# Performance work log

Measured on AMD Instinct MI355X. Metric: run time of the kernel, lower is better.

## Reference

```python
import jax, jax.numpy as jnp
import numpy as np

OUT_FEATURES = 4096
IN_FEATURES = 4096

# NF4 codebook (bitsandbytes normal-float 4-bit values)
_NF4_CODEBOOK = np.array([
    -1.0, -0.6961928, -0.52507305, -0.3949175, -0.28444138, -0.18477343,
    -0.09105004, 0.0, 0.0795803, 0.1609302, 0.2461123, 0.33791524,
    0.44070983, 0.562617, 0.72295684, 1.0], dtype=np.float32)


def setup_inputs() -> dict:
    key = jax.random.key(0)
    k_x, k_codes, k_scale, k_bias = jax.random.split(key, 4)
    x = jax.random.normal(k_x, (4, 2048, IN_FEATURES), dtype=jnp.float32)
    # packed uint8 nibble codes stored as int32 in [0, 256)
    packed_codes = jax.random.randint(
        k_codes, (OUT_FEATURES * IN_FEATURES // 2,), 0, 256, dtype=jnp.int32)
    # positive per-channel scales [out, 1]
    scale = jax.random.uniform(k_scale, (OUT_FEATURES, 1), dtype=jnp.float32) * 0.05 + 0.01
    bias = jax.random.normal(k_bias, (OUT_FEATURES,), dtype=jnp.float32)
    return {"x": x, "packed_codes": packed_codes, "scale": scale, "bias": bias}


def _dequantize_nf4(packed_codes, scale):
    codebook = jnp.asarray(_NF4_CODEBOOK)
    low = packed_codes & 15           # even positions
    high = (packed_codes >> 4) & 15   # odd positions
    # interleave: unpacked[0::2]=low, unpacked[1::2]=high
    idx = jnp.stack([low, high], axis=-1).reshape(-1)  # [out*in]
    w = codebook[idx].reshape(OUT_FEATURES, IN_FEATURES) * scale  # [out, in]
    return w


def reference(x, packed_codes, scale, bias):
    w = _dequantize_nf4(packed_codes, scale)
    # F.linear: x @ w.T + bias
    return jnp.einsum("bsi,oi->bso", x, w) + bias
```

## Files before the change

kernel.cpp:

```cpp
#include <hip/hip_runtime.h>
#include <stdint.h>

#define IN_F 4096
#define OUT_F 4096
#define M_ROWS 8192

__device__ __constant__ int c_nf4_i8[16] = {
    -127, -88, -67, -50, -36, -23, -12, 0, 10, 20, 31, 43, 56, 71, 92, 127};

typedef int i32x4 __attribute__((ext_vector_type(4)));
typedef int i32x16 __attribute__((ext_vector_type(16)));

__global__ __launch_bounds__(256) void k_quant_x(
    const float* __restrict__ x, signed char* __restrict__ xq,
    float* __restrict__ steps) {
  const int row = blockIdx.x;
  const int tid = threadIdx.x;
  const float4* xr = (const float4*)(x + (size_t)row * IN_F);
  float4 v[4];
  float m = 0.0f;
#pragma unroll
  for (int i = 0; i < 4; ++i) {
    v[i] = xr[tid + 256 * i];
    m = fmaxf(m, fmaxf(fmaxf(fabsf(v[i].x), fabsf(v[i].y)),
                       fmaxf(fabsf(v[i].z), fabsf(v[i].w))));
  }
#pragma unroll
  for (int off = 32; off > 0; off >>= 1) m = fmaxf(m, __shfl_xor(m, off));
  __shared__ float wmax[4];
  if ((tid & 63) == 0) wmax[tid >> 6] = m;
  __syncthreads();
  m = fmaxf(fmaxf(wmax[0], wmax[1]), fmaxf(wmax[2], wmax[3]));
  const float inv = (m > 0.0f) ? 127.0f / m : 0.0f;
  if (tid == 0) steps[row] = m * (1.0f / 127.0f);
  int* oq = (int*)(xq + (size_t)row * IN_F);
#pragma unroll
  for (int i = 0; i < 4; ++i) {
    int q0 = (int)rintf(v[i].x * inv);
    int q1 = (int)rintf(v[i].y * inv);
    int q2 = (int)rintf(v[i].z * inv);
    int q3 = (int)rintf(v[i].w * inv);
    oq[tid + 256 * i] =
        (q0 & 255) | ((q1 & 255) << 8) | ((q2 & 255) << 16) | (q3 << 24);
  }
}

__global__ __launch_bounds__(256) void k_dequant(
    const int* __restrict__ packed, signed char* __restrict__ W) {
  __shared__ short lut[256];
  {
    const int b = threadIdx.x;
    const int lo = c_nf4_i8[b & 15], hi = c_nf4_i8[b >> 4];
    lut[b] = (short)((lo & 0xFF) | ((hi & 0xFF) << 8));
  }
  __syncthreads();
  const int tid = blockIdx.x * 256 + threadIdx.x;
  const int4 ca = ((const int4*)packed)[2 * tid];
  const int4 cb = ((const int4*)packed)[2 * tid + 1];
  union { short h[8]; int4 v; } o;
  o.h[0] = lut[ca.x]; o.h[1] = lut[ca.y]; o.h[2] = lut[ca.z]; o.h[3] = lut[ca.w];
  o.h[4] = lut[cb.x]; o.h[5] = lut[cb.y]; o.h[6] = lut[cb.z]; o.h[7] = lut[cb.w];
  ((int4*)W)[tid] = o.v;
}

#define GLL(gptr, lptr)                                          \
  __builtin_amdgcn_global_load_lds(                              \
      (__attribute__((address_space(1))) void*)(gptr),           \
      (__attribute__((address_space(3))) void*)(lptr), 16, 0, 0)

__global__ __launch_bounds__(256) void k_gemm(
    const signed char* __restrict__ A,
    const signed char* __restrict__ B,
    const float* __restrict__ steps,
    const float* __restrict__ scale,
    const float* __restrict__ bias,
    float* __restrict__ C) {
  __shared__ __align__(16) signed char sA[128 * 128];
  __shared__ __align__(16) signed char sB[128 * 128];
  const int tid = threadIdx.x;
  const int lane = tid & 63;
  const int w  = tid >> 6;
  const int wm = w >> 1;
  const int wn = w & 1;
  const int bm = blockIdx.y * 128;
  const int bn = blockIdx.x * 128;

  i32x16 acc[2][2] = {};

  const int srow  = w * 32 + (lane >> 3);
  const int schnk = (lane & 7) ^ (lane >> 3);
  const signed char* gA = A + (size_t)(bm + srow) * IN_F + schnk * 16;
  const signed char* gB = B + (size_t)(bn + srow) * IN_F + schnk * 16;
  signed char* lA = sA + w * 32 * 128;
  signed char* lB = sB + w * 32 * 128;

  const int r31   = lane & 31;
  const int khalf = lane >> 5;
  const int rx7   = lane & 7;

  for (int k0 = 0; k0 < IN_F; k0 += 128) {
#pragma unroll
    for (int g = 0; g < 4; ++g) {
      GLL(gA + k0 + g * 8 * IN_F, lA + g * 1024);
      GLL(gB + k0 + g * 8 * IN_F, lB + g * 1024);
    }
    __syncthreads();
#pragma unroll
    for (int ks = 0; ks < 4; ++ks) {
      const int ch = ((2 * ks + khalf) ^ rx7) * 16;
      i32x4 a0 = *(const i32x4*)&sA[(wm * 64      + r31) * 128 + ch];
      i32x4 a1 = *(const i32x4*)&sA[(wm * 64 + 32 + r31) * 128 + ch];
      i32x4 b0 = *(const i32x4*)&sB[(wn * 64      + r31) * 128 + ch];
      i32x4 b1 = *(const i32x4*)&sB[(wn * 64 + 32 + r31) * 128 + ch];
      acc[0][0] = __builtin_amdgcn_mfma_i32_32x32x32_i8(a0, b0, acc[0][0], 0, 0, 0);
      acc[0][1] = __builtin_amdgcn_mfma_i32_32x32x32_i8(a0, b1, acc[0][1], 0, 0, 0);
      acc[1][0] = __builtin_amdgcn_mfma_i32_32x32x32_i8(a1, b0, acc[1][0], 0, 0, 0);
      acc[1][1] = __builtin_amdgcn_mfma_i32_32x32x32_i8(a1, b1, acc[1][1], 0, 0, 0);
    }
    __syncthreads();
  }

  const int colb = bn + wn * 64 + r31;
  const int rowb = bm + wm * 64 + 4 * khalf;
#pragma unroll
  for (int fj = 0; fj < 2; ++fj) {
    const int col = colb + fj * 32;
    const float fc = scale[col] * (1.0f / 127.0f);
    const float bv = bias[col];
#pragma unroll
    for (int fi = 0; fi < 2; ++fi) {
      const int row0 = rowb + fi * 32;
#pragma unroll
      for (int reg = 0; reg < 16; ++reg) {
        const int row = row0 + (reg & 3) + 8 * (reg >> 2);
        C[(size_t)row * OUT_F + col] =
            (float)acc[fi][fj][reg] * (steps[row] * fc) + bv;
      }
    }
  }
}

extern "C" void kernel_launch(void* const* d_in, const int* in_sizes, int n_in,
                              void* d_out, int out_size, void* d_ws, size_t ws_size,
                              hipStream_t stream) {
  const float* x      = (const float*)d_in[0];
  const int* packed   = (const int*)d_in[1];
  const float* scale  = (const float*)d_in[2];
  const float* bias   = (const float*)d_in[3];
  float* out = (float*)d_out;

  signed char* Xq = (signed char*)d_ws;
  signed char* Wq = Xq + (size_t)M_ROWS * IN_F;
  float* steps = (float*)(Wq + (size_t)OUT_F * IN_F);

  k_quant_x<<<M_ROWS, 256, 0, stream>>>(x, Xq, steps);
  k_dequant<<<(OUT_F * IN_F / 2) / (256 * 8), 256, 0, stream>>>(packed, Wq);
  dim3 grid(OUT_F / 128, M_ROWS / 128);
  k_gemm<<<grid, 256, 0, stream>>>(Xq, Wq, steps, scale, bias, out);
}
```

Before: 397.9 us.

## Restructure int8 GEMM into 256x256 tiles with double-buffered staged LDS pipeline

Rewrites the int8 MFMA GEMM to use 512-thread blocks computing 256x256 output tiles, with double-buffered LDS, and splits each K tile into eight quadrant phases. Each phase interleaves async global-to-LDS loads for the next tile with MFMA work, using explicit barriers, vmcnt waits and s_setprio. It also adds a block-index swizzle for L2 locality. The aim is to hide global load latency and raise arithmetic intensity per byte of LDS traffic. The cost is 128KB of LDS per block and a fragile hand-ordered wait schedule.

```diff
diff --git a/kernel.cpp b/kernel.cpp
--- a/kernel.cpp
+++ b/kernel.cpp
@@ -68,73 +68,144 @@
       (__attribute__((address_space(1))) void*)(gptr),           \
       (__attribute__((address_space(3))) void*)(lptr), 16, 0, 0)
 
-__global__ __launch_bounds__(256) void k_gemm(
+#define FENCE() asm volatile("" ::: "memory")
+
+__device__ __forceinline__ void gemm_phase(
+    const signed char* SA, const signed char* SB, int mh, int nh,
+    int wm, int wn, int r31, int khalf, int ln7, int w,
+    i32x16& acc0, i32x16& acc1,
+    const signed char* gsrc, signed char* ldst, int kt, int doStage,
+    int waitMode) {
+  i32x4 a0[4], a1[4], b[4];
+#pragma unroll
+  for (int ks = 0; ks < 4; ++ks) {
+    const int ch = ((2 * ks + khalf) ^ ln7) * 16;
+    a0[ks] = *(const i32x4*)&SA[(wm * 64 + mh * 128 + r31) * 128 + ch];
+    a1[ks] = *(const i32x4*)&SA[(wm * 64 + mh * 128 + 32 + r31) * 128 + ch];
+    b[ks]  = *(const i32x4*)&SB[(wn * 32 + nh * 128 + r31) * 128 + ch];
+  }
+  if (doStage) {
+#pragma unroll
+    for (int g = 0; g < 2; ++g)
+      GLL(gsrc + (size_t)(g * 64) * IN_F + (size_t)kt * 128,
+          ldst + (g * 64 + w * 8) * 128);
+  }
+  FENCE();
+  __builtin_amdgcn_s_barrier();
+  FENCE();
+  __builtin_amdgcn_s_setprio(1);
+#pragma unroll
+  for (int ks = 0; ks < 4; ++ks) {
+    acc0 = __builtin_amdgcn_mfma_i32_32x32x32_i8(a0[ks], b[ks], acc0, 0, 0, 0);
+    acc1 = __builtin_amdgcn_mfma_i32_32x32x32_i8(a1[ks], b[ks], acc1, 0, 0, 0);
+  }
+  __builtin_amdgcn_s_setprio(0);
+  if (waitMode == 1) {
+    asm volatile("s_waitcnt vmcnt(4)" ::: "memory");
+  } else if (waitMode == 2) {
+    asm volatile("s_waitcnt vmcnt(0)" ::: "memory");
+  }
+  FENCE();
+  __builtin_amdgcn_s_barrier();
+  FENCE();
+}
+
+__global__ __launch_bounds__(512, 2) void k_gemm(
     const signed char* __restrict__ A,
     const signed char* __restrict__ B,
     const float* __restrict__ steps,
     const float* __restrict__ scale,
     const float* __restrict__ bias,
     float* __restrict__ C) {
-  __shared__ __align__(16) signed char sA[128 * 128];
-  __shared__ __align__(16) signed char sB[128 * 128];
+  __shared__ __align__(16) signed char sA[2][256 * 128];
+  __shared__ __align__(16) signed char sB[2][256 * 128];
   const int tid = threadIdx.x;
   const int lane = tid & 63;
-  const int w  = tid >> 6;
-  const int wm = w >> 1;
-  const int wn = w & 1;
-  const int bm = blockIdx.y * 128;
-  const int bn = blockIdx.x * 128;
-
-  i32x16 acc[2][2] = {};
-
-  const int srow  = w * 32 + (lane >> 3);
+  const int w = tid >> 6;
+  const int wm = w >> 2;
+  const int wn = w & 3;
+  const int r31 = lane & 31;
+  const int khalf = lane >> 5;
+  const int ln7 = lane & 7;
+
+  const int orig = blockIdx.x;
+  const int swz = (orig & 7) * 64 + (orig >> 3);
+  const int bn = (swz & 15) * 256;
+  const int bm = (swz >> 4) * 256;
+
+  const int tr = w * 8 + (lane >> 3);
   const int schnk = (lane & 7) ^ (lane >> 3);
-  const signed char* gA = A + (size_t)(bm + srow) * IN_F + schnk * 16;
-  const signed char* gB = B + (size_t)(bn + srow) * IN_F + schnk * 16;
-  signed char* lA = sA + w * 32 * 128;
-  signed char* lB = sB + w * 32 * 128;
-
-  const int r31   = lane & 31;
-  const int khalf = lane >> 5;
-  const int rx7   = lane & 7;
-
-  for (int k0 = 0; k0 < IN_F; k0 += 128) {
-#pragma unroll
-    for (int g = 0; g < 4; ++g) {
-      GLL(gA + k0 + g * 8 * IN_F, lA + g * 1024);
-      GLL(gB + k0 + g * 8 * IN_F, lB + g * 1024);
-    }
-    __syncthreads();
-#pragma unroll
-    for (int ks = 0; ks < 4; ++ks) {
-      const int ch = ((2 * ks + khalf) ^ rx7) * 16;
-      i32x4 a0 = *(const i32x4*)&sA[(wm * 64      + r31) * 128 + ch];
-      i32x4 a1 = *(const i32x4*)&sA[(wm * 64 + 32 + r31) * 128 + ch];
-      i32x4 b0 = *(const i32x4*)&sB[(wn * 64      + r31) * 128 + ch];
-      i32x4 b1 = *(const i32x4*)&sB[(wn * 64 + 32 + r31) * 128 + ch];
-      acc[0][0] = __builtin_amdgcn_mfma_i32_32x32x32_i8(a0, b0, acc[0][0], 0, 0, 0);
-      acc[0][1] = __builtin_amdgcn_mfma_i32_32x32x32_i8(a0, b1, acc[0][1], 0, 0, 0);
-      acc[1][0] = __builtin_amdgcn_mfma_i32_32x32x32_i8(a1, b0, acc[1][0], 0, 0, 0);
-      acc[1][1] = __builtin_amdgcn_mfma_i32_32x32x32_i8(a1, b1, acc[1][1], 0, 0, 0);
-    }
-    __syncthreads();
-  }
-
-  const int colb = bn + wn * 64 + r31;
-  const int rowb = bm + wm * 64 + 4 * khalf;
-#pragma unroll
-  for (int fj = 0; fj < 2; ++fj) {
-    const int col = colb + fj * 32;
-    const float fc = scale[col] * (1.0f / 127.0f);
-    const float bv = bias[col];
-#pragma unroll
-    for (int fi = 0; fi < 2; ++fi) {
-      const int row0 = rowb + fi * 32;
-#pragma unroll
-      for (int reg = 0; reg < 16; ++reg) {
-        const int row = row0 + (reg & 3) + 8 * (reg >> 2);
-        C[(size_t)row * OUT_F + col] =
-            (float)acc[fi][fj][reg] * (steps[row] * fc) + bv;
+  const signed char* gA = A + (size_t)(bm + tr) * IN_F + schnk * 16;
+  const signed char* gB = B + (size_t)(bn + tr) * IN_F + schnk * 16;
+
+  i32x16 acc[2][2][2] = {};
+
+  auto stage2 = [&](const signed char* gsrc, signed char* ldst, int kt) {
+#pragma unroll
+    for (int g = 0; g < 2; ++g)
+      GLL(gsrc + (size_t)(g * 64) * IN_F + (size_t)kt * 128,
+          ldst + (g * 64 + w * 8) * 128);
+  };
+
+  stage2(gA, &sA[0][0], 0);
+  stage2(gA + (size_t)128 * IN_F, &sA[0][128 * 128], 0);
+  stage2(gB, &sB[0][0], 0);
+  stage2(gB + (size_t)128 * IN_F, &sB[0][128 * 128], 0);
+  stage2(gA, &sA[1][0], 1);
+  stage2(gB, &sB[1][0], 1);
+  asm volatile("s_waitcnt vmcnt(4)" ::: "memory");
+  FENCE();
+  __builtin_amdgcn_s_barrier();
+  FENCE();
+
+#pragma unroll 1
+  for (int it = 0; it < 16; ++it) {
+    const int nl = (it < 15) ? 1 : 0;
+    const int kY = 2 * it + 1;
+    const int kXn = 2 * it + 2;
+    const int kYn = 2 * it + 3;
+    gemm_phase(sA[0], sB[0], 0, 0, wm, wn, r31, khalf, ln7, w,
+               acc[0][0][0], acc[0][1][0],
+               gA + (size_t)128 * IN_F, &sA[1][128 * 128], kY, 1, 0);
+    gemm_phase(sA[0], sB[0], 0, 1, wm, wn, r31, khalf, ln7, w,
+               acc[0][0][1], acc[0][1][1],
+               gB + (size_t)128 * IN_F, &sB[1][128 * 128], kY, 1, 0);
+    gemm_phase(sA[0], sB[0], 1, 0, wm, wn, r31, khalf, ln7, w,
+               acc[1][0][0], acc[1][1][0],
+               gA, &sA[0][0], kXn, nl, 0);
+    gemm_phase(sA[0], sB[0], 1, 1, wm, wn, r31, khalf, ln7, w,
+               acc[1][0][1], acc[1][1][1],
+               gB, &sB[0][0], kXn, nl, nl ? 1 : 2);
+    gemm_phase(sA[1], sB[1], 0, 0, wm, wn, r31, khalf, ln7, w,
+               acc[0][0][0], acc[0][1][0],
+               gA + (size_t)128 * IN_F, &sA[0][128 * 128], kXn, nl, 0);
+    gemm_phase(sA[1], sB[1], 0, 1, wm, wn, r31, khalf, ln7, w,
+               acc[0][0][1], acc[0][1][1],
+               gB + (size_t)128 * IN_F, &sB[0][128 * 128], kXn, nl, 0);
+    gemm_phase(sA[1], sB[1], 1, 0, wm, wn, r31, khalf, ln7, w,
+               acc[1][0][0], acc[1][1][0],
+               gA, &sA[1][0], kYn, nl, 0);
+    gemm_phase(sA[1], sB[1], 1, 1, wm, wn, r31, khalf, ln7, w,
+               acc[1][0][1], acc[1][1][1],
+               gB, &sB[1][0], kYn, nl, nl ? 1 : 0);
+  }
+
+#pragma unroll
+  for (int mh = 0; mh < 2; ++mh) {
+#pragma unroll
+    for (int f = 0; f < 2; ++f) {
+      const int row0 = bm + wm * 64 + mh * 128 + f * 32 + 4 * khalf;
+#pragma unroll
+      for (int nh = 0; nh < 2; ++nh) {
+        const int col = bn + wn * 32 + nh * 128 + r31;
+        const float fc = scale[col] * (1.0f / 127.0f);
+        const float bv = bias[col];
+#pragma unroll
+        for (int reg = 0; reg < 16; ++reg) {
+          const int row = row0 + (reg & 3) + 8 * (reg >> 2);
+          C[(size_t)row * OUT_F + col] =
+              (float)acc[mh][f][nh][reg] * (steps[row] * fc) + bv;
+        }
       }
     }
   }
@@ -155,6 +226,6 @@
 
   k_quant_x<<<M_ROWS, 256, 0, stream>>>(x, Xq, steps);
   k_dequant<<<(OUT_F * IN_F / 2) / (256 * 8), 256, 0, stream>>>(packed, Wq);
-  dim3 grid(OUT_F / 128, M_ROWS / 128);
-  k_gemm<<<grid, 256, 0, stream>>>(Xq, Wq, steps, scale, bias, out);
-}
+  k_gemm<<<(OUT_F / 256) * (M_ROWS / 256), 512, 0, stream>>>(
+      Xq, Wq, steps, scale, bias, out);
+}
```

After: 423.4 us. +6.4%, slower.
